# Optimization experiments

Hardware: AMD Instinct MI355X
Metric: run time of the kernel (lower is better)

## Reference

```python
import jax, jax.numpy as jnp
import numpy as np

DIM = 768
HID = 3072  # 4 * DIM
EPS = 1e-5


def layer_norm(x, w, b):
    mu = jnp.mean(x, axis=-1, keepdims=True)
    var = jnp.var(x, axis=-1, keepdims=True)
    return (x - mu) * jax.lax.rsqrt(var + EPS) * w + b


def setup_inputs() -> dict:
    key = jax.random.key(0)
    ks = jax.random.split(key, 8)
    C, H = DIM, HID
    s = lambda fan_in: 1.0 / np.sqrt(fan_in)
    return {
        "x": jax.random.normal(ks[0], (32, 577, C), dtype=jnp.float32),
        "norm1_w": jnp.ones((C,), jnp.float32),
        "norm1_b": jnp.zeros((C,), jnp.float32),
        "qkv_w": jax.random.uniform(ks[1], (3 * C, C), jnp.float32, -s(C), s(C)),
        "proj_w": jax.random.uniform(ks[2], (C, C), jnp.float32, -s(C), s(C)),
        "proj_b": jax.random.uniform(ks[3], (C,), jnp.float32, -s(C), s(C)),
        "norm2_w": jnp.ones((C,), jnp.float32),
        "norm2_b": jnp.zeros((C,), jnp.float32),
        "fc1_w": jax.random.uniform(ks[4], (H, C), jnp.float32, -s(C), s(C)),
        "fc1_b": jax.random.uniform(ks[5], (H,), jnp.float32, -s(C), s(C)),
        "fc2_w": jax.random.uniform(ks[6], (C, H), jnp.float32, -s(H), s(H)),
        "fc2_b": jax.random.uniform(ks[7], (C,), jnp.float32, -s(H), s(H)),
    }


def reference(x, norm1_w, norm1_b, qkv_w, proj_w, proj_b,
              norm2_w, norm2_b, fc1_w, fc1_b, fc2_w, fc2_b):
    B, N, C = x.shape
    attn_size = int((N - 1) ** 0.5)
    scale = C ** -0.5

    # --- Attention on norm1(x) (single head) ---
    h = layer_norm(x, norm1_w, norm1_b)
    qkv = (h @ qkv_w.T).reshape(B, N, 3, C)           # [B,N,3,C]
    q, k, v = qkv[:, :, 0], qkv[:, :, 1], qkv[:, :, 2]
    attn = jax.nn.softmax(jnp.einsum('bnc,bmc->bnm', q, k) * scale, axis=-1)
    y = jnp.einsum('bnm,bmc->bnc', attn, v)           # [B,N,C]
    # Faithful to torch: .transpose(1,2).reshape(B,N,C) scrambles layout
    y = jnp.transpose(y, (0, 2, 1)).reshape(B, N, C)
    a = y @ proj_w.T + proj_b
    token_attn = attn[:, 0, 1:].reshape(B, 1, attn_size, attn_size)

    # Faithful to torch Block: input residual is discarded, attention out doubled
    x = a + a

    # --- MLP (exact GELU, as nn.GELU default) ---
    m = layer_norm(x, norm2_w, norm2_b)
    m = jax.nn.gelu(m @ fc1_w.T + fc1_b, approximate=False)
    m = m @ fc2_w.T + fc2_b
    x = x + m
    return (x, token_attn)
```

## Files before the change

### kernel.cpp

```cpp
#include <hip/hip_runtime.h>
#include <hip/hip_bf16.h>

#define Bz   32
#define Nn_  577
#define Np   640
#define Cc   768
#define Hh   3072
#define Mrows (Bz * Nn_)
#define OUT_X (Mrows * Cc)
#define SCALE 0.03608439182435161f

typedef unsigned short ushort_t;
typedef short short8 __attribute__((ext_vector_type(8)));
typedef float f32x4 __attribute__((ext_vector_type(4)));

__device__ __forceinline__ ushort_t f2b(float f) {
    __hip_bfloat16 h = __float2bfloat16(f);
    return *reinterpret_cast<ushort_t*>(&h);
}

__device__ __forceinline__ void gl16(const ushort_t* g, ushort_t* l) {
    __builtin_amdgcn_global_load_lds(
        (const __attribute__((address_space(1))) void*)g,
        (__attribute__((address_space(3))) void*)l, 16, 0, 0);
}

__device__ __forceinline__ float bsum(float v, float* sm) {
    #pragma unroll
    for (int o = 32; o > 0; o >>= 1) v += __shfl_down(v, o, 64);
    int lane = threadIdx.x & 63, wid = threadIdx.x >> 6;
    if (lane == 0) sm[wid] = v;
    __syncthreads();
    float r = sm[0] + sm[1] + sm[2] + sm[3];
    __syncthreads();
    return r;
}
__device__ __forceinline__ float bmax(float v, float* sm) {
    #pragma unroll
    for (int o = 32; o > 0; o >>= 1) v = fmaxf(v, __shfl_down(v, o, 64));
    int lane = threadIdx.x & 63, wid = threadIdx.x >> 6;
    if (lane == 0) sm[wid] = v;
    __syncthreads();
    float r = fmaxf(fmaxf(sm[0], sm[1]), fmaxf(sm[2], sm[3]));
    __syncthreads();
    return r;
}

__global__ void cvt_kernel(const float* __restrict__ in, ushort_t* __restrict__ out, int n) {
    int i = blockIdx.x * 256 + threadIdx.x;
    if (i < n) out[i] = f2b(in[i]);
}

__global__ void ln_bf16(const float* __restrict__ x, const float* __restrict__ w,
                        const float* __restrict__ b, ushort_t* __restrict__ out) {
    __shared__ float sm[8];
    long long row = blockIdx.x;
    const float* xr = x + row * Cc;
    float v[3]; float s = 0.f;
    #pragma unroll
    for (int i = 0; i < 3; ++i) { v[i] = xr[threadIdx.x + i * 256]; s += v[i]; }
    float mu = bsum(s, sm) * (1.f / (float)Cc);
    float sq = 0.f;
    #pragma unroll
    for (int i = 0; i < 3; ++i) { float d = v[i] - mu; sq += d * d; }
    float var = bsum(sq, sm + 4) * (1.f / (float)Cc);
    float inv = rsqrtf(var + 1e-5f);
    ushort_t* orow = out + row * Cc;
    #pragma unroll
    for (int i = 0; i < 3; ++i) {
        int c = threadIdx.x + i * 256;
        orow[c] = f2b((v[i] - mu) * inv * w[c] + b[c]);
    }
}

__global__ void softmax_bf16(const float* __restrict__ Sf, ushort_t* __restrict__ Sb,
                             float* __restrict__ tok) {
    __shared__ float sm[8];
    long long row = blockIdx.x;
    int b_l = (int)(row / Nn_), r = (int)(row - (long long)b_l * Nn_);
    const float* src = Sf + row * Np;
    ushort_t* dst = Sb + row * Np;
    float v[3]; float mx = -1e30f;
    #pragma unroll
    for (int i = 0; i < 3; ++i) {
        int c = threadIdx.x + i * 256;
        v[i] = (c < Nn_) ? src[c] : -1e30f;
        mx = fmaxf(mx, v[i]);
    }
    mx = bmax(mx, sm);
    float s = 0.f;
    #pragma unroll
    for (int i = 0; i < 3; ++i) {
        int c = threadIdx.x + i * 256;
        v[i] = (c < Nn_) ? expf(v[i] - mx) : 0.f;
        s += v[i];
    }
    s = bsum(s, sm + 4);
    float inv = 1.f / s;
    #pragma unroll
    for (int i = 0; i < 3; ++i) {
        int c = threadIdx.x + i * 256;
        float p = v[i] * inv;
        if (c < Np) dst[c] = (c < Nn_) ? f2b(p) : (ushort_t)0;
        if (r == 0 && c >= 1 && c < Nn_) tok[(long long)b_l * 576 + (c - 1)] = p;
    }
}

#define EPS_STORE  0
#define EPS_X2     1
#define EPS_GELU   2
#define EPS_ADD    3
#define EPS_QKV    4

#define MM_STAGE(AS, BS, k0) do {            \
    gl16(Ag0 + (k0), &AS[e0]);               \
    gl16(Ag1 + (k0), &AS[e1]);               \
    gl16(Bg0 + (k0), &BS[e0]);               \
    gl16(Bg1 + (k0), &BS[e1]);               \
} while (0)

#define MM_COMPUTE(AS, BS) do {                                             \
    short8 af[4], bfr[4];                                                   \
    _Pragma("unroll")                                                       \
    for (int i = 0; i < 4; ++i) {                                           \
        int r = wr + i * 16 + fr;                                           \
        af[i] = *(const short8*)&AS[r * 32 + ((kq ^ (r & 3)) << 3)];        \
    }                                                                       \
    _Pragma("unroll")                                                       \
    for (int j = 0; j < 4; ++j) {                                           \
        int r = wc + j * 16 + fr;                                           \
        bfr[j] = *(const short8*)&BS[r * 32 + ((kq ^ (r & 3)) << 3)];       \
    }                                                                       \
    _Pragma("unroll")                                                       \
    for (int i = 0; i < 4; ++i)                                             \
        _Pragma("unroll")                                                   \
        for (int j = 0; j < 4; ++j)                                         \
            acc[i][j] = __builtin_amdgcn_mfma_f32_16x16x32_bf16(            \
                af[i], bfr[j], acc[i][j], 0, 0, 0);                         \
} while (0)

template<int EPI, typename OutT>
__global__ __launch_bounds__(256)
void mm_bf16(const ushort_t* __restrict__ A, long long sAb, int lda, int M,
             const ushort_t* __restrict__ B, long long sBb, int ldb, int Nv,
             const float* __restrict__ bias,
             OutT* __restrict__ O, long long sOb, int ldo,
             int K, float alpha,
             ushort_t* __restrict__ qQ, ushort_t* __restrict__ qK, ushort_t* __restrict__ qV)
{
    __shared__ __align__(16) ushort_t As0[128 * 32];
    __shared__ __align__(16) ushort_t As1[128 * 32];
    __shared__ __align__(16) ushort_t Bs0[128 * 32];
    __shared__ __align__(16) ushort_t Bs1[128 * 32];
    const int z = blockIdx.z;
    A += (long long)z * sAb; B += (long long)z * sBb;
    if (O) O += (long long)z * sOb;
    const int n0 = blockIdx.x * 128;
    const int m0 = blockIdx.y * 128;
    const int tid = threadIdx.x;
    const int lane = tid & 63;
    const int wv = tid >> 6;
    const int wr = (wv >> 1) << 6;
    const int wc = (wv & 1) << 6;
    const int fr = lane & 15;
    const int kq = lane >> 4;

    const int e0 = tid * 8, e1 = 2048 + tid * 8;
    const int ra0 = e0 >> 5, qa0 = (((e0 & 31) >> 3) ^ (ra0 & 3)) << 3;
    const int ra1 = e1 >> 5, qa1 = (((e1 & 31) >> 3) ^ (ra1 & 3)) << 3;
    const ushort_t* Ag0 = A + (long long)min(m0 + ra0, M - 1) * lda + qa0;
    const ushort_t* Ag1 = A + (long long)min(m0 + ra1, M - 1) * lda + qa1;
    const ushort_t* Bg0 = B + (long long)min(n0 + ra0, Nv - 1) * ldb + qa0;
    const ushort_t* Bg1 = B + (long long)min(n0 + ra1, Nv - 1) * ldb + qa1;

    f32x4 acc[4][4] = {};

    const int nt = K >> 5;

    MM_STAGE(As0, Bs0, 0);
    __syncthreads();

    for (int t = 0; t < nt; t += 2) {
        MM_STAGE(As1, Bs1, (t + 1) << 5);
        MM_COMPUTE(As0, Bs0);
        __syncthreads();
        if (t + 2 < nt) MM_STAGE(As0, Bs0, (t + 2) << 5);
        MM_COMPUTE(As1, Bs1);
        __syncthreads();
    }

    #pragma unroll
    for (int i = 0; i < 4; ++i) {
        int mb = m0 + wr + i * 16 + (lane >> 4) * 4;
        #pragma unroll
        for (int j = 0; j < 4; ++j) {
            int n = n0 + wc + j * 16 + fr;
            if (n >= Nv) continue;
            f32x4 v4 = acc[i][j];
            #pragma unroll
            for (int r = 0; r < 4; ++r) {
                int m = mb + r;
                if (m >= M) continue;
                float v = v4[r] * alpha;
                if constexpr (EPI == EPS_QKV) {
                    int b_l = m / Nn_, rr = m - b_l * Nn_;
                    if (n < Cc)            qQ[(long long)m * Cc + n] = f2b(v);
                    else if (n < 2 * Cc)   qK[(long long)m * Cc + (n - Cc)] = f2b(v);
                    else                   qV[((long long)b_l * Cc + (n - 2 * Cc)) * Np + rr] = f2b(v);
                } else if constexpr (EPI == EPS_ADD) {
                    if (bias) v += bias[n];
                    long long oi = (long long)m * ldo + n;
                    O[oi] += v;
                } else {
                    if (bias) v += bias[n];
                    if constexpr (EPI == EPS_X2) v *= 2.f;
                    if constexpr (EPI == EPS_GELU) v = 0.5f * v * (1.f + erff(v * 0.70710678118654752f));
                    long long oi = (long long)m * ldo + n;
                    if constexpr (sizeof(OutT) == 2) O[oi] = (OutT)f2b(v);
                    else                             O[oi] = (OutT)v;
                }
            }
        }
    }
}

#define STAGE256(LA, LB, kt) do {                                   \
    _Pragma("unroll")                                               \
    for (int j = 0; j < 4; ++j) gl16(Ag[j] + (kt) * 64, &LA[j * 4096 + sdst]); \
    _Pragma("unroll")                                               \
    for (int j = 0; j < 4; ++j) gl16(Bg[j] + (kt) * 64, &LB[j * 4096 + sdst]); \
} while (0)

#define COMPUTE256(LA, LB) do {                                                   \
    short8 bfv[4][2];                                                             \
    _Pragma("unroll")                                                             \
    for (int nf = 0; nf < 4; ++nf) {                                              \
        int rb = (wn64 + nf * 16 + fr) * 64;                                      \
        bfv[nf][0] = *(const short8*)&LB[rb + ck0];                               \
        bfv[nf][1] = *(const short8*)&LB[rb + ck1];                               \
    }                                                                             \
    _Pragma("unroll")                                                             \
    for (int mh = 0; mh < 4; ++mh) {                                              \
        int ra0 = (wm128 + mh * 32 + fr) * 64;                                    \
        int ra1 = (wm128 + mh * 32 + 16 + fr) * 64;                               \
        short8 a00 = *(const short8*)&LA[ra0 + ck0];                              \
        short8 a01 = *(const short8*)&LA[ra0 + ck1];                              \
        short8 a10 = *(const short8*)&LA[ra1 + ck0];                              \
        short8 a11 = *(const short8*)&LA[ra1 + ck1];                              \
        __builtin_amdgcn_s_setprio(1);                                            \
        _Pragma("unroll")                                                         \
        for (int nf = 0; nf < 4; ++nf) {                                          \
            acc[mh*2][nf]   = __builtin_amdgcn_mfma_f32_16x16x32_bf16(a00, bfv[nf][0], acc[mh*2][nf],   0,0,0); \
            acc[mh*2][nf]   = __builtin_amdgcn_mfma_f32_16x16x32_bf16(a01, bfv[nf][1], acc[mh*2][nf],   0,0,0); \
            acc[mh*2+1][nf] = __builtin_amdgcn_mfma_f32_16x16x32_bf16(a10, bfv[nf][0], acc[mh*2+1][nf], 0,0,0); \
            acc[mh*2+1][nf] = __builtin_amdgcn_mfma_f32_16x16x32_bf16(a11, bfv[nf][1], acc[mh*2+1][nf], 0,0,0); \
        }                                                                         \
        __builtin_amdgcn_s_setprio(0);                                            \
    }                                                                             \
} while (0)

#define TILE_STEP256(RA, RB, WA, WB, kt) do {                       \
    if ((kt) + 1 < nt) {                                            \
        STAGE256(WA, WB, (kt) + 1);                                 \
        asm volatile("s_waitcnt vmcnt(8)" ::: "memory");            \
    } else {                                                        \
        asm volatile("s_waitcnt vmcnt(0)" ::: "memory");            \
    }                                                               \
    __builtin_amdgcn_s_barrier();                                   \
    __builtin_amdgcn_sched_barrier(0);                              \
    COMPUTE256(RA, RB);                                             \
    __builtin_amdgcn_s_barrier();                                   \
    __builtin_amdgcn_sched_barrier(0);                              \
} while (0)

template<int EPI, typename OutT>
__global__ __launch_bounds__(512, 2)
void mm256(const ushort_t* __restrict__ A, int lda, int M,
           const ushort_t* __restrict__ B, int ldb, int Nv,
           const float* __restrict__ bias,
           OutT* __restrict__ O, int ldo,
           int K, float alpha,
           ushort_t* __restrict__ qQ, ushort_t* __restrict__ qK, ushort_t* __restrict__ qV)
{
    __shared__ __align__(16) ushort_t As0[256 * 64];
    __shared__ __align__(16) ushort_t Bs0[256 * 64];
    __shared__ __align__(16) ushort_t As1[256 * 64];
    __shared__ __align__(16) ushort_t Bs1[256 * 64];

    const int nwg = gridDim.x * gridDim.y;
    const int flat = blockIdx.y * gridDim.x + blockIdx.x;
    const int qq = nwg >> 3, rr8 = nwg & 7;
    const int xcd = flat & 7, idx = flat >> 3;
    const int wg = (xcd < rr8 ? xcd * (qq + 1) : rr8 * (qq + 1) + (xcd - rr8) * qq) + idx;
    const int bx = wg % gridDim.x, by = wg / gridDim.x;

    const int n0 = bx * 256, m0 = by * 256;
    const int tid = (int)threadIdx.x;
    const int lane = tid & 63;
    const int wv = tid >> 6;
    const int wm128 = (wv >> 2) * 128;
    const int wn64  = (wv & 3) * 64;
    const int fr = lane & 15;
    const int kq = lane >> 4;
    const int f7 = fr & 7;
    const int ck0 = (kq ^ f7) * 8;
    const int ck1 = ((4 + kq) ^ f7) * 8;

    const int srow = tid >> 3;
    const int schunk = (tid & 7) ^ (srow & 7);
    const int sdst = tid * 8;
    const ushort_t* Ag[4];
    const ushort_t* Bg[4];
    #pragma unroll
    for (int j = 0; j < 4; ++j) {
        Ag[j] = A + (long long)min(m0 + j * 64 + srow, M - 1) * lda + schunk * 8;
        Bg[j] = B + (long long)min(n0 + j * 64 + srow, Nv - 1) * ldb + schunk * 8;
    }

    f32x4 acc[8][4] = {};
    const int nt = K >> 6;

    STAGE256(As0, Bs0, 0);

    for (int t = 0; t < nt; t += 2) {
        TILE_STEP256(As0, Bs0, As1, Bs1, t);
        TILE_STEP256(As1, Bs1, As0, Bs0, t + 1);
    }

    #pragma unroll
    for (int mf = 0; mf < 8; ++mf) {
        int mb = m0 + wm128 + mf * 16 + (lane >> 4) * 4;
        #pragma unroll
        for (int nf = 0; nf < 4; ++nf) {
            int n = n0 + wn64 + nf * 16 + fr;
            if (n >= Nv) continue;
            f32x4 v4 = acc[mf][nf];
            #pragma unroll
            for (int r = 0; r < 4; ++r) {
                int m = mb + r;
                if (m >= M) continue;
                float v = v4[r] * alpha;
                if constexpr (EPI == EPS_QKV) {
                    int b_l = m / Nn_, rq = m - b_l * Nn_;
                    if (n < Cc)            qQ[(long long)m * Cc + n] = f2b(v);
                    else if (n < 2 * Cc)   qK[(long long)m * Cc + (n - Cc)] = f2b(v);
                    else                   qV[((long long)b_l * Cc + (n - 2 * Cc)) * Np + rq] = f2b(v);
                } else if constexpr (EPI == EPS_ADD) {
                    if (bias) v += bias[n];
                    long long oi = (long long)m * ldo + n;
                    O[oi] += v;
                } else {
                    if (bias) v += bias[n];
                    if constexpr (EPI == EPS_X2) v *= 2.f;
                    if constexpr (EPI == EPS_GELU) v = 0.5f * v * (1.f + erff(v * 0.70710678118654752f));
                    long long oi = (long long)m * ldo + n;
                    if constexpr (sizeof(OutT) == 2) O[oi] = (OutT)f2b(v);
                    else                             O[oi] = (OutT)v;
                }
            }
        }
    }
}

extern "C" void kernel_launch(void* const* d_in, const int* in_sizes, int n_in,
                              void* d_out, int out_size, void* d_ws, size_t ws_size,
                              hipStream_t stream) {
    const float* x      = (const float*)d_in[0];
    const float* n1w    = (const float*)d_in[1];
    const float* n1b    = (const float*)d_in[2];
    const float* qkv_w  = (const float*)d_in[3];
    const float* proj_w = (const float*)d_in[4];
    const float* proj_b = (const float*)d_in[5];
    const float* n2w    = (const float*)d_in[6];
    const float* n2b    = (const float*)d_in[7];
    const float* fc1w   = (const float*)d_in[8];
    const float* fc1b   = (const float*)d_in[9];
    const float* fc2w   = (const float*)d_in[10];
    const float* fc2b   = (const float*)d_in[11];
    float* out = (float*)d_out;
    float* x2  = out;
    float* tok = out + OUT_X;

    char* ws = (char*)d_ws;
    const long long nWq = (long long)3 * Cc * Cc;
    const long long nWp = (long long)Cc * Cc;
    const long long nW1 = (long long)Hh * Cc;
    const long long nW2 = (long long)Cc * Hh;
    ushort_t* wq = (ushort_t*)ws;
    ushort_t* wp = wq + nWq;
    ushort_t* w1 = wp + nWp;
    ushort_t* w2 = w1 + nW1;
    const long long WBYTES = 2 * (nWq + nWp + nW1 + nW2);
    char* dyn = ws + WBYTES;
    long long avail = (long long)ws_size - WBYTES;

    const long long perG = 3LL * Nn_ * Cc * 2 + (long long)Cc * Np * 2
                         + (long long)Nn_ * Np * 4 + (long long)Nn_ * Np * 2;
    int G = 1;
    { const int o[6] = {32, 16, 8, 4, 2, 1};
      for (int i = 0; i < 6; ++i) if ((long long)o[i] * perG <= avail) { G = o[i]; break; } }
    int CH = Nn_;
    { const int o[6] = {32, 16, 8, 4, 2, 1};
      for (int i = 0; i < 6; ++i) if ((long long)o[i] * Nn_ * (Cc + Hh) * 2 <= avail) { CH = o[i] * Nn_; break; } }

    ushort_t* hbf = (ushort_t*)dyn;
    ushort_t* Q   = hbf + (long long)G * Nn_ * Cc;
    ushort_t* Kb  = Q   + (long long)G * Nn_ * Cc;
    ushort_t* Vt  = Kb  + (long long)G * Nn_ * Cc;
    float*    Sf  = (float*)(Vt + (long long)G * Cc * Np);
    ushort_t* Sb  = (ushort_t*)(Sf + (long long)G * Nn_ * Np);
    ushort_t* Yt  = hbf;
    ushort_t* g = (ushort_t*)dyn;
    ushort_t* t = g + (long long)CH * Cc;

    cvt_kernel<<<(int)((nWq + 255) / 256), 256, 0, stream>>>(qkv_w, wq, (int)nWq);
    cvt_kernel<<<(int)((nWp + 255) / 256), 256, 0, stream>>>(proj_w, wp, (int)nWp);
    cvt_kernel<<<(int)((nW1 + 255) / 256), 256, 0, stream>>>(fc1w, w1, (int)nW1);
    cvt_kernel<<<(int)((nW2 + 255) / 256), 256, 0, stream>>>(fc2w, w2, (int)nW2);

    for (int b0 = 0; b0 < Bz; b0 += G) {
        const int MR = G * Nn_;
        const int myM256 = (MR + 255) / 256;

        ln_bf16<<<MR, 256, 0, stream>>>(x + (long long)b0 * Nn_ * Cc, n1w, n1b, hbf);

        mm256<EPS_QKV, float><<<dim3(9, myM256, 1), 512, 0, stream>>>(
            hbf, Cc, MR, wq, Cc, 3 * Cc, nullptr,
            (float*)nullptr, 0, Cc, 1.f, Q, Kb, Vt);

        mm_bf16<EPS_STORE, float><<<dim3(5, 5, G), 256, 0, stream>>>(
            Q, (long long)Nn_ * Cc, Cc, Nn_, Kb, (long long)Nn_ * Cc, Cc, Nn_, nullptr,
            Sf, (long long)Nn_ * Np, Np, Cc, SCALE, nullptr, nullptr, nullptr);

        softmax_bf16<<<MR, 256, 0, stream>>>(Sf, Sb, tok + (long long)b0 * 576);

        mm_bf16<EPS_STORE, ushort_t><<<dim3(5, 6, G), 256, 0, stream>>>(
            Vt, (long long)Cc * Np, Np, Cc, Sb, (long long)Nn_ * Np, Np, Nn_, nullptr,
            Yt, (long long)Cc * Nn_, Nn_, Np, 1.f, nullptr, nullptr, nullptr);

        mm256<EPS_X2, float><<<dim3(3, myM256, 1), 512, 0, stream>>>(
            Yt, Cc, MR, wp, Cc, Cc, proj_b,
            x2 + (long long)b0 * Nn_ * Cc, Cc, Cc, 1.f, nullptr, nullptr, nullptr);
    }

    for (int c0 = 0; c0 < Mrows; c0 += CH) {
        const int cn = (Mrows - c0 < CH) ? (Mrows - c0) : CH;
        const int myC256 = (cn + 255) / 256;

        ln_bf16<<<cn, 256, 0, stream>>>(x2 + (long long)c0 * Cc, n2w, n2b, g);

        mm256<EPS_GELU, ushort_t><<<dim3(12, myC256, 1), 512, 0, stream>>>(
            g, Cc, cn, w1, Cc, Hh, fc1b,
            t, Hh, Cc, 1.f, nullptr, nullptr, nullptr);

        mm256<EPS_ADD, float><<<dim3(3, myC256, 1), 512, 0, stream>>>(
            t, Hh, cn, w2, Hh, Cc, fc2b,
            x2 + (long long)c0 * Cc, Cc, Hh, 1.f, nullptr, nullptr, nullptr);
    }
}
```

Measured before the change: 872.1 us.

## Restructure 256-tile GEMM into four-phase half-K pipeline and use fast GELU

```diff
diff --git a/kernel.cpp b/kernel.cpp
--- a/kernel.cpp
+++ b/kernel.cpp
@@ -17,6 +17,18 @@
 __device__ __forceinline__ ushort_t f2b(float f) {
     __hip_bfloat16 h = __float2bfloat16(f);
     return *reinterpret_cast<ushort_t*>(&h);
+}
+
+__device__ __forceinline__ float gelu_f(float v) {
+    float z  = v * 0.70710678118654752f;
+    float az = fabsf(z);
+    float t_ = __builtin_amdgcn_rcpf(1.f + 0.3275911f * az);
+    float y  = t_ * (0.254829592f + t_ * (-0.284496736f + t_ * (1.421413741f +
+               t_ * (-1.453152027f + t_ * 1.061405429f))));
+    float e  = __expf(-az * az);
+    float er = 1.f - y * e;
+    er = (z < 0.f) ? -er : er;
+    return 0.5f * v * (1.f + er);
 }
 
 __device__ __forceinline__ void gl16(const ushort_t* g, ushort_t* l) {
@@ -174,7 +186,6 @@
     const ushort_t* Bg1 = B + (long long)min(n0 + ra1, Nv - 1) * ldb + qa1;
 
     f32x4 acc[4][4] = {};
-
     const int nt = K >> 5;
 
     MM_STAGE(As0, Bs0, 0);
@@ -214,7 +225,7 @@
                 } else {
                     if (bias) v += bias[n];
                     if constexpr (EPI == EPS_X2) v *= 2.f;
-                    if constexpr (EPI == EPS_GELU) v = 0.5f * v * (1.f + erff(v * 0.70710678118654752f));
+                    if constexpr (EPI == EPS_GELU) v = gelu_f(v);
                     long long oi = (long long)m * ldo + n;
                     if constexpr (sizeof(OutT) == 2) O[oi] = (OutT)f2b(v);
                     else                             O[oi] = (OutT)v;
@@ -224,57 +235,48 @@
     }
 }
 
-#define STAGE256(LA, LB, kt) do {                                   \
-    _Pragma("unroll")                                               \
-    for (int j = 0; j < 4; ++j) gl16(Ag[j] + (kt) * 64, &LA[j * 4096 + sdst]); \
-    _Pragma("unroll")                                               \
-    for (int j = 0; j < 4; ++j) gl16(Bg[j] + (kt) * 64, &LB[j * 4096 + sdst]); \
-} while (0)
-
-#define COMPUTE256(LA, LB) do {                                                   \
-    short8 bfv[4][2];                                                             \
-    _Pragma("unroll")                                                             \
-    for (int nf = 0; nf < 4; ++nf) {                                              \
-        int rb = (wn64 + nf * 16 + fr) * 64;                                      \
-        bfv[nf][0] = *(const short8*)&LB[rb + ck0];                               \
-        bfv[nf][1] = *(const short8*)&LB[rb + ck1];                               \
-    }                                                                             \
-    _Pragma("unroll")                                                             \
-    for (int mh = 0; mh < 4; ++mh) {                                              \
-        int ra0 = (wm128 + mh * 32 + fr) * 64;                                    \
-        int ra1 = (wm128 + mh * 32 + 16 + fr) * 64;                               \
-        short8 a00 = *(const short8*)&LA[ra0 + ck0];                              \
-        short8 a01 = *(const short8*)&LA[ra0 + ck1];                              \
-        short8 a10 = *(const short8*)&LA[ra1 + ck0];                              \
-        short8 a11 = *(const short8*)&LA[ra1 + ck1];                              \
-        __builtin_amdgcn_s_setprio(1);                                            \
-        _Pragma("unroll")                                                         \
-        for (int nf = 0; nf < 4; ++nf) {                                          \
-            acc[mh*2][nf]   = __builtin_amdgcn_mfma_f32_16x16x32_bf16(a00, bfv[nf][0], acc[mh*2][nf],   0,0,0); \
-            acc[mh*2][nf]   = __builtin_amdgcn_mfma_f32_16x16x32_bf16(a01, bfv[nf][1], acc[mh*2][nf],   0,0,0); \
-            acc[mh*2+1][nf] = __builtin_amdgcn_mfma_f32_16x16x32_bf16(a10, bfv[nf][0], acc[mh*2+1][nf], 0,0,0); \
-            acc[mh*2+1][nf] = __builtin_amdgcn_mfma_f32_16x16x32_bf16(a11, bfv[nf][1], acc[mh*2+1][nf], 0,0,0); \
-        }                                                                         \
-        __builtin_amdgcn_s_setprio(0);                                            \
-    }                                                                             \
-} while (0)
-
-#define TILE_STEP256(RA, RB, WA, WB, kt) do {                       \
-    if ((kt) + 1 < nt) {                                            \
-        STAGE256(WA, WB, (kt) + 1);                                 \
-        asm volatile("s_waitcnt vmcnt(8)" ::: "memory");            \
-    } else {                                                        \
-        asm volatile("s_waitcnt vmcnt(0)" ::: "memory");            \
-    }                                                               \
-    __builtin_amdgcn_s_barrier();                                   \
-    __builtin_amdgcn_sched_barrier(0);                              \
-    COMPUTE256(RA, RB);                                             \
-    __builtin_amdgcn_s_barrier();                                   \
-    __builtin_amdgcn_sched_barrier(0);                              \
+#define STAGE8(P, h, tt) do {                                        \
+    const int ko_ = (tt) * 64 + ((h) >> 1) * 32;                     \
+    if (((h) & 1) == 0) {                                            \
+        gl16(AsS0 + ko_, &HA[P][(h) >> 1][s0 * 8]);                  \
+        gl16(AsS1 + ko_, &HA[P][(h) >> 1][s1 * 8]);                  \
+    } else {                                                         \
+        gl16(BsS0 + ko_, &HB[P][(h) >> 1][s0 * 8]);                  \
+        gl16(BsS1 + ko_, &HB[P][(h) >> 1][s1 * 8]);                  \
+    }                                                                \
+} while (0)
+
+#define LDA4(P, ks, fbase) do {                                      \
+    _Pragma("unroll")                                                \
+    for (int f_ = 0; f_ < 4; ++f_)                                   \
+        av[f_] = *(const short8*)&HA[P][ks][abase + ((fbase) + f_) * 512]; \
+} while (0)
+
+#define LDB4(P, ks) do {                                             \
+    _Pragma("unroll")                                                \
+    for (int n_ = 0; n_ < 4; ++n_)                                   \
+        bv[n_] = *(const short8*)&HB[P][ks][bbase + n_ * 512];       \
+} while (0)
+
+#define MFMA16(fbase) do {                                           \
+    __builtin_amdgcn_s_setprio(1);                                   \
+    _Pragma("unroll")                                                \
+    for (int f_ = 0; f_ < 4; ++f_)                                   \
+        _Pragma("unroll")                                            \
+        for (int n_ = 0; n_ < 4; ++n_)                               \
+            acc[(fbase) + f_][n_] = __builtin_amdgcn_mfma_f32_16x16x32_bf16( \
+                av[f_], bv[n_], acc[(fbase) + f_][n_], 0, 0, 0);     \
+    __builtin_amdgcn_s_setprio(0);                                   \
+} while (0)
+
+#define PH_SYNC() do {                                               \
+    __builtin_amdgcn_s_barrier();                                    \
+    asm volatile("s_waitcnt lgkmcnt(0)" ::: "memory");               \
+    __builtin_amdgcn_sched_barrier(0);                               \
 } while (0)
 
 template<int EPI, typename OutT>
-__global__ __launch_bounds__(512, 2)
+__global__ __launch_bounds__(512, 1)
 void mm256(const ushort_t* __restrict__ A, int lda, int M,
            const ushort_t* __restrict__ B, int ldb, int Nv,
            const float* __restrict__ bias,
@@ -282,10 +284,8 @@
            int K, float alpha,
            ushort_t* __restrict__ qQ, ushort_t* __restrict__ qK, ushort_t* __restrict__ qV)
 {
-    __shared__ __align__(16) ushort_t As0[256 * 64];
-    __shared__ __align__(16) ushort_t Bs0[256 * 64];
-    __shared__ __align__(16) ushort_t As1[256 * 64];
-    __shared__ __align__(16) ushort_t Bs1[256 * 64];
+    __shared__ __align__(16) ushort_t HA[2][2][8192];
+    __shared__ __align__(16) ushort_t HB[2][2][8192];
 
     const int nwg = gridDim.x * gridDim.y;
     const int flat = blockIdx.y * gridDim.x + blockIdx.x;
@@ -302,29 +302,58 @@
     const int wn64  = (wv & 3) * 64;
     const int fr = lane & 15;
     const int kq = lane >> 4;
-    const int f7 = fr & 7;
-    const int ck0 = (kq ^ f7) * 8;
-    const int ck1 = ((4 + kq) ^ f7) * 8;
-
-    const int srow = tid >> 3;
-    const int schunk = (tid & 7) ^ (srow & 7);
-    const int sdst = tid * 8;
-    const ushort_t* Ag[4];
-    const ushort_t* Bg[4];
-    #pragma unroll
-    for (int j = 0; j < 4; ++j) {
-        Ag[j] = A + (long long)min(m0 + j * 64 + srow, M - 1) * lda + schunk * 8;
-        Bg[j] = B + (long long)min(n0 + j * 64 + srow, Nv - 1) * ldb + schunk * 8;
-    }
+
+    const int sl    = (kq + 4 * (fr & 1)) ^ (fr >> 1);
+    const int lref  = (fr >> 1) * 64 + sl * 8;
+    const int abase = wm128 * 32 + lref;
+    const int bbase = wn64 * 32 + lref;
+
+    const int s0 = tid, s1 = tid + 512;
+    const int line0 = tid >> 3;
+    const int u0 = (tid & 7) ^ (line0 & 7);
+    const int r0 = (line0 << 1) | (u0 >> 2);
+    const int c0 = u0 & 3;
+    const ushort_t* AsS0 = A + (long long)min(m0 + r0,       M - 1) * lda + c0 * 8;
+    const ushort_t* AsS1 = A + (long long)min(m0 + r0 + 128, M - 1) * lda + c0 * 8;
+    const ushort_t* BsS0 = B + (long long)min(n0 + r0,       Nv - 1) * ldb + c0 * 8;
+    const ushort_t* BsS1 = B + (long long)min(n0 + r0 + 128, Nv - 1) * ldb + c0 * 8;
 
     f32x4 acc[8][4] = {};
     const int nt = K >> 6;
 
-    STAGE256(As0, Bs0, 0);
-
-    for (int t = 0; t < nt; t += 2) {
-        TILE_STEP256(As0, Bs0, As1, Bs1, t);
-        TILE_STEP256(As1, Bs1, As0, Bs0, t + 1);
+    STAGE8(0, 0, 0); STAGE8(0, 1, 0); STAGE8(0, 2, 0); STAGE8(0, 3, 0);
+    asm volatile("s_waitcnt vmcnt(4)" ::: "memory");
+    __builtin_amdgcn_s_barrier();
+
+    for (int t = 0; t < nt; ++t) {
+        const int P = t & 1, Q = P ^ 1;
+        const bool pf = (t + 1 < nt);
+        short8 av[4], bv[4];
+
+        LDA4(P, 0, 0); LDB4(P, 0);
+        if (pf) STAGE8(Q, 0, t + 1);
+        PH_SYNC();
+        MFMA16(0);
+        __builtin_amdgcn_s_barrier();
+
+        LDA4(P, 0, 4);
+        if (pf) { STAGE8(Q, 1, t + 1); asm volatile("s_waitcnt vmcnt(4)" ::: "memory"); }
+        else    {                      asm volatile("s_waitcnt vmcnt(0)" ::: "memory"); }
+        PH_SYNC();
+        MFMA16(4);
+        __builtin_amdgcn_s_barrier();
+
+        LDA4(P, 1, 0); LDB4(P, 1);
+        if (pf) STAGE8(Q, 2, t + 1);
+        PH_SYNC();
+        MFMA16(0);
+        __builtin_amdgcn_s_barrier();
+
+        LDA4(P, 1, 4);
+        if (pf) { STAGE8(Q, 3, t + 1); asm volatile("s_waitcnt vmcnt(4)" ::: "memory"); }
+        PH_SYNC();
+        MFMA16(4);
+        __builtin_amdgcn_s_barrier();
     }
 
     #pragma unroll
@@ -352,7 +381,7 @@
                 } else {
                     if (bias) v += bias[n];
                     if constexpr (EPI == EPS_X2) v *= 2.f;
-                    if constexpr (EPI == EPS_GELU) v = 0.5f * v * (1.f + erff(v * 0.70710678118654752f));
+                    if constexpr (EPI == EPS_GELU) v = gelu_f(v);
                     long long oi = (long long)m * ldo + n;
                     if constexpr (sizeof(OutT) == 2) O[oi] = (OutT)f2b(v);
                     else                             O[oi] = (OutT)v;
@@ -426,7 +455,7 @@
 
         mm256<EPS_QKV, float><<<dim3(9, myM256, 1), 512, 0, stream>>>(
             hbf, Cc, MR, wq, Cc, 3 * Cc, nullptr,
-            (float*)nullptr, 0, Cc, 1.f, Q, Kb, Vt);
+            (float*)nullptr, Cc, Cc, 1.f, Q, Kb, Vt);
 
         mm_bf16<EPS_STORE, float><<<dim3(5, 5, G), 256, 0, stream>>>(
             Q, (long long)Nn_ * Cc, Cc, Nn_, Kb, (long long)Nn_ * Cc, Cc, Nn_, nullptr,
```

New measurement: 859.6 us. About the same (-1.4%).
